# Kernel tuning notes

Hardware: AMD Instinct MI355X
Metric: run time of the kernel (lower is better)

Reference implementation:

```python
import jax, jax.numpy as jnp
import numpy as np

TEMPERATURE = 0.1
EPS = 1e-8  # torch CosineSimilarity eps


def _l2_normalize(x):
    # torch cosine sim: x / max(||x||, eps)
    n = jnp.sqrt(jnp.sum(x * x, axis=1, keepdims=True))
    return x / jnp.maximum(n, EPS)


def _pairwise_softmax(zx, zy):
    # cosine similarity matrix [N, N]: sim[i, j] = cos(zx[i], zy[j])
    sim = _l2_normalize(zx) @ _l2_normalize(zy).T  # [N, N]
    # softmax over dim=1 (columns) after temperature scaling
    return jax.nn.softmax(sim / TEMPERATURE, axis=1)


def _kl_div_mean(log_p, q):
    # torch F.kl_div(input=log_p, target=q, reduction='mean'):
    # mean over ALL elements of q * (log(q) - log_p)
    return jnp.mean(q * (jnp.log(q) - log_p))


def setup_inputs() -> dict:
    key = jax.random.key(0)
    k1, k2, k3, k4 = jax.random.split(key, 4)
    N, D = 4096, 768
    return {
        "zxs": jax.random.normal(k1, (N, D), dtype=jnp.float32),
        "zys": jax.random.normal(k2, (N, D), dtype=jnp.float32),
        "zxt": jax.random.normal(k3, (N, D), dtype=jnp.float32),
        "zyt": jax.random.normal(k4, (N, D), dtype=jnp.float32),
    }


def reference(zxs, zys, zxt, zyt):
    sim_s = _pairwise_softmax(zxs, zys)  # [N, N]
    sim_t = _pairwise_softmax(zxt, zyt)  # [N, N]
    loss_s = _kl_div_mean(jnp.log(sim_s), jax.lax.stop_gradient(sim_t))
    loss_t = _kl_div_mean(jnp.log(sim_t), jax.lax.stop_gradient(sim_s))
    return (loss_s, loss_t)
```

## Files before the change

kernel.cpp:

```cpp
#include <hip/hip_runtime.h>
#include <hip/hip_bf16.h>

#define N 4096
#define D 768
#define NK 24

typedef float f32x4 __attribute__((ext_vector_type(4)));
typedef unsigned long u64x2 __attribute__((ext_vector_type(2)));

typedef __attribute__((address_space(3))) unsigned int as3_uint;
typedef const __attribute__((address_space(1))) unsigned int as1_uint;

__device__ __forceinline__ void gload16(const void* g, void* l) {
    __builtin_amdgcn_global_load_lds((as1_uint*)g, (as3_uint*)l, 16, 0, 0);
}


__global__ __launch_bounds__(256) void norm4(const float* __restrict__ x0,
                                             const float* __restrict__ x1,
                                             const float* __restrict__ x2,
                                             const float* __restrict__ x3,
                                             unsigned char* __restrict__ o) {
    int a = blockIdx.y;
    const float* x = (a == 0) ? x0 : (a == 1) ? x1 : (a == 2) ? x2 : x3;
    unsigned char* out = o + (size_t)a * N * D;
    int i0 = blockIdx.x * 32;
    __shared__ __align__(16) unsigned char tile[24576];
    int t = threadIdx.x, lane = t & 63, w = t >> 6;

    for (int rr = 0; rr < 8; ++rr) {
        int R = i0 + w * 8 + rr;
        const f32x4* xr = (const f32x4*)(x + (size_t)R * D);
        f32x4 v0 = xr[lane * 2], v1 = xr[lane * 2 + 1];
        f32x4 v2 = {}, v3 = {};
        if (lane < 32) { v2 = xr[128 + lane * 2]; v3 = xr[128 + lane * 2 + 1]; }
        float ss = v0[0]*v0[0] + v0[1]*v0[1] + v0[2]*v0[2] + v0[3]*v0[3]
                 + v1[0]*v1[0] + v1[1]*v1[1] + v1[2]*v1[2] + v1[3]*v1[3]
                 + v2[0]*v2[0] + v2[1]*v2[1] + v2[2]*v2[2] + v2[3]*v2[3]
                 + v3[0]*v3[0] + v3[1]*v3[1] + v3[2]*v3[2] + v3[3]*v3[3];
        #pragma unroll
        for (int m = 1; m < 64; m <<= 1) ss += __shfl_xor(ss, m);
        float s = 1.0f / fmaxf(sqrtf(ss), 1e-8f);

        {
            unsigned int wlo = __builtin_amdgcn_cvt_pk_fp8_f32(v0[0]*s, v0[1]*s, 0, false) & 0xffff;
            unsigned int whi = __builtin_amdgcn_cvt_pk_fp8_f32(v0[2]*s, v0[3]*s, 0, false) & 0xffff;
            unsigned int w0 = wlo | (whi << 16);
            wlo = __builtin_amdgcn_cvt_pk_fp8_f32(v1[0]*s, v1[1]*s, 0, false) & 0xffff;
            whi = __builtin_amdgcn_cvt_pk_fp8_f32(v1[2]*s, v1[3]*s, 0, false) & 0xffff;
            unsigned int w1 = wlo | (whi << 16);
            int g = lane;
            int off = (g >> 2) * 1024 + ((R & 15) + ((g & 3) << 4)) * 16 + (((R >> 4) & 1) << 3);
            *(uint2*)(tile + off) = make_uint2(w0, w1);
        }
        if (lane < 32) {
            unsigned int wlo = __builtin_amdgcn_cvt_pk_fp8_f32(v2[0]*s, v2[1]*s, 0, false) & 0xffff;
            unsigned int whi = __builtin_amdgcn_cvt_pk_fp8_f32(v2[2]*s, v2[3]*s, 0, false) & 0xffff;
            unsigned int w0 = wlo | (whi << 16);
            wlo = __builtin_amdgcn_cvt_pk_fp8_f32(v3[0]*s, v3[1]*s, 0, false) & 0xffff;
            whi = __builtin_amdgcn_cvt_pk_fp8_f32(v3[2]*s, v3[3]*s, 0, false) & 0xffff;
            unsigned int w1 = wlo | (whi << 16);
            int g = 64 + lane;
            int off = (g >> 2) * 1024 + ((R & 15) + ((g & 3) << 4)) * 16 + (((R >> 4) & 1) << 3);
            *(uint2*)(tile + off) = make_uint2(w0, w1);
        }
    }
    __syncthreads();
    unsigned char* dst = out + (size_t)(i0 >> 5) * 24576;
    #pragma unroll
    for (int i = 0; i < 6; ++i)
        ((int4*)dst)[t + i * 256] = ((const int4*)tile)[t + i * 256];
}


__global__ __launch_bounds__(256, 2) void fused_gemm(
        const unsigned char* __restrict__ Xs, const unsigned char* __restrict__ Ys,
        const unsigned char* __restrict__ Xt, const unsigned char* __restrict__ Yt,
        float* __restrict__ partial) {
    __shared__ __align__(16) char smem[32768];
    const int t = threadIdx.x;
    const int jb = blockIdx.x, ib = blockIdx.y;
    const int i0 = ib * 128;
    const int lane = t & 63, wid = t >> 6;
    const int wm = wid >> 1, wn = wid & 1;

    f32x4 acc_s[4][4] = {};
    f32x4 acc_t[4][4] = {};

    const size_t srcA = ((size_t)(ib * 4 + (t >> 6))) * 24576 + (size_t)(t & 63) * 16;
    const size_t srcB = ((size_t)(jb * 4 + (t >> 6))) * 24576 + (size_t)(t & 63) * 16;
    const unsigned char* gAs = Xs + srcA;
    const unsigned char* gAt = Xt + srcA;
    const unsigned char* gBs = Ys + srcB;
    const unsigned char* gBt = Yt + srcB;

    char* cur = smem;
    char* nxt = smem + 16384;
    const int sdst = t * 16;

    gload16(gAs, cur + sdst);
    gload16(gBs, cur + 8192 + sdst);
    gload16(gAt, cur + 4096 + sdst);
    gload16(gBt, cur + 12288 + sdst);
    gAs += 1024; gBs += 1024; gAt += 1024; gBt += 1024;

    const int offA = wm * 2048 + lane * 16;
    const int offB = 8192 + wn * 2048 + lane * 16;

    #pragma unroll 1
    for (int kt = 0; kt < NK - 1; ++kt) {
        asm volatile("s_waitcnt vmcnt(2)" ::: "memory");
        __builtin_amdgcn_s_barrier();
        u64x2 a01 = *(const u64x2*)(cur + offA);
        u64x2 a23 = *(const u64x2*)(cur + offA + 1024);
        u64x2 b01 = *(const u64x2*)(cur + offB);
        u64x2 b23 = *(const u64x2*)(cur + offB + 1024);
        gload16(gAs, nxt + sdst);
        gload16(gBs, nxt + 8192 + sdst);
        gAs += 1024; gBs += 1024;
        {
            long a[4] = {(long)a01[0], (long)a01[1], (long)a23[0], (long)a23[1]};
            long b[4] = {(long)b01[0], (long)b01[1], (long)b23[0], (long)b23[1]};
            __builtin_amdgcn_s_setprio(1);
            #pragma unroll
            for (int m = 0; m < 4; ++m)
                #pragma unroll
                for (int n = 0; n < 4; ++n)
                    acc_s[m][n] = __builtin_amdgcn_mfma_f32_16x16x32_fp8_fp8(a[m], b[n], acc_s[m][n], 0, 0, 0);
            __builtin_amdgcn_s_setprio(0);
        }

        asm volatile("s_waitcnt vmcnt(2)" ::: "memory");
        __builtin_amdgcn_s_barrier();
        a01 = *(const u64x2*)(cur + 4096 + offA);
        a23 = *(const u64x2*)(cur + 4096 + offA + 1024);
        b01 = *(const u64x2*)(cur + 4096 + offB);
        b23 = *(const u64x2*)(cur + 4096 + offB + 1024);
        gload16(gAt, nxt + 4096 + sdst);
        gload16(gBt, nxt + 12288 + sdst);
        gAt += 1024; gBt += 1024;
        {
            long a[4] = {(long)a01[0], (long)a01[1], (long)a23[0], (long)a23[1]};
            long b[4] = {(long)b01[0], (long)b01[1], (long)b23[0], (long)b23[1]};
            __builtin_amdgcn_s_setprio(1);
            #pragma unroll
            for (int m = 0; m < 4; ++m)
                #pragma unroll
                for (int n = 0; n < 4; ++n)
                    acc_t[m][n] = __builtin_amdgcn_mfma_f32_16x16x32_fp8_fp8(a[m], b[n], acc_t[m][n], 0, 0, 0);
            __builtin_amdgcn_s_setprio(0);
        }

        char* tmp = cur; cur = nxt; nxt = tmp;
    }

    asm volatile("s_waitcnt vmcnt(2)" ::: "memory");
    __builtin_amdgcn_s_barrier();
    {
        u64x2 a01 = *(const u64x2*)(cur + offA);
        u64x2 a23 = *(const u64x2*)(cur + offA + 1024);
        u64x2 b01 = *(const u64x2*)(cur + offB);
        u64x2 b23 = *(const u64x2*)(cur + offB + 1024);
        long a[4] = {(long)a01[0], (long)a01[1], (long)a23[0], (long)a23[1]};
        long b[4] = {(long)b01[0], (long)b01[1], (long)b23[0], (long)b23[1]};
        __builtin_amdgcn_s_setprio(1);
        #pragma unroll
        for (int m = 0; m < 4; ++m)
            #pragma unroll
            for (int n = 0; n < 4; ++n)
                acc_s[m][n] = __builtin_amdgcn_mfma_f32_16x16x32_fp8_fp8(a[m], b[n], acc_s[m][n], 0, 0, 0);
        __builtin_amdgcn_s_setprio(0);
    }
    asm volatile("s_waitcnt vmcnt(0)" ::: "memory");
    __builtin_amdgcn_s_barrier();
    {
        u64x2 a01 = *(const u64x2*)(cur + 4096 + offA);
        u64x2 a23 = *(const u64x2*)(cur + 4096 + offA + 1024);
        u64x2 b01 = *(const u64x2*)(cur + 4096 + offB);
        u64x2 b23 = *(const u64x2*)(cur + 4096 + offB + 1024);
        long a[4] = {(long)a01[0], (long)a01[1], (long)a23[0], (long)a23[1]};
        long b[4] = {(long)b01[0], (long)b01[1], (long)b23[0], (long)b23[1]};
        __builtin_amdgcn_s_setprio(1);
        #pragma unroll
        for (int m = 0; m < 4; ++m)
            #pragma unroll
            for (int n = 0; n < 4; ++n)
                acc_t[m][n] = __builtin_amdgcn_mfma_f32_16x16x32_fp8_fp8(a[m], b[n], acc_t[m][n], 0, 0, 0);
        __builtin_amdgcn_s_setprio(0);
    }

    __syncthreads();
    float* part = (float*)smem;
    int g = lane >> 4, cl = lane & 15;

    #pragma unroll
    for (int m = 0; m < 4; ++m) {
        float st[4][4];
        #pragma unroll
        for (int r = 0; r < 4; ++r) { st[r][0] = 0.f; st[r][1] = 0.f; st[r][2] = 0.f; st[r][3] = 0.f; }
        #pragma unroll
        for (int n = 0; n < 4; ++n)
            #pragma unroll
            for (int r = 0; r < 4; ++r) {
                float ls = 10.0f * acc_s[m][n][r];
                float lt = 10.0f * acc_t[m][n][r];
                float es = __expf(ls - 10.0f);
                float et = __expf(lt - 10.0f);
                st[r][0] += es;
                st[r][1] += et;
                st[r][2] += es * (ls - lt);
                st[r][3] += et * (lt - ls);
            }
        #pragma unroll
        for (int r = 0; r < 4; ++r)
            #pragma unroll
            for (int s = 0; s < 4; ++s) {
                float v = st[r][s];
                v += __shfl_xor(v, 1);
                v += __shfl_xor(v, 2);
                v += __shfl_xor(v, 4);
                v += __shfl_xor(v, 8);
                st[r][s] = v;
            }
        if (cl == 0) {
            int row = wm * 64 + m * 16 + g * 4;
            #pragma unroll
            for (int r = 0; r < 4; ++r)
                #pragma unroll
                for (int s = 0; s < 4; ++s)
                    part[(wn * 128 + row + r) * 4 + s] = st[r][s];
        }
    }
    __syncthreads();
    #pragma unroll
    for (int q = 0; q < 2; ++q) {
        int idx = t + q * 256;
        int row = idx >> 2, s = idx & 3;
        float v = part[(0 * 128 + row) * 4 + s] + part[(1 * 128 + row) * 4 + s];
        partial[((size_t)jb * N + (i0 + row)) * 4 + s] = v;
    }
}

__global__ __launch_bounds__(256) void reduce_rows(const float* __restrict__ partial,
                                                   float* __restrict__ blocksum) {
    int row = blockIdx.x * 256 + threadIdx.x;
    float zs = 0.f, zt = 0.f, ws = 0.f, wt = 0.f;
    for (int jb = 0; jb < 32; ++jb) {
        const float* p = partial + ((size_t)jb * N + row) * 4;
        zs += p[0]; zt += p[1]; ws += p[2]; wt += p[3];
    }
    float ls_row = wt / zt - logf(zt) + logf(zs);
    float lt_row = ws / zs - logf(zs) + logf(zt);
    #pragma unroll
    for (int m = 1; m < 64; m <<= 1) {
        ls_row += __shfl_xor(ls_row, m);
        lt_row += __shfl_xor(lt_row, m);
    }
    __shared__ float rs[4], rt[4];
    int lane = threadIdx.x & 63, wid = threadIdx.x >> 6;
    if (lane == 0) { rs[wid] = ls_row; rt[wid] = lt_row; }
    __syncthreads();
    if (threadIdx.x == 0) {
        blocksum[blockIdx.x * 2]     = rs[0] + rs[1] + rs[2] + rs[3];
        blocksum[blockIdx.x * 2 + 1] = rt[0] + rt[1] + rt[2] + rt[3];
    }
}

__global__ void final_reduce(const float* __restrict__ blocksum, float* __restrict__ out) {
    float a = 0.f, b = 0.f;
    if (threadIdx.x < 16) { a = blocksum[threadIdx.x * 2]; b = blocksum[threadIdx.x * 2 + 1]; }
    #pragma unroll
    for (int m = 1; m < 16; m <<= 1) { a += __shfl_xor(a, m); b += __shfl_xor(b, m); }
    if (threadIdx.x == 0) {
        const float inv = 1.0f / 16777216.0f;
        out[0] = a * inv;
        out[1] = b * inv;
    }
}

extern "C" void kernel_launch(void* const* d_in, const int* in_sizes, int n_in,
                              void* d_out, int out_size, void* d_ws, size_t ws_size,
                              hipStream_t stream) {
    const float* zxs = (const float*)d_in[0];
    const float* zys = (const float*)d_in[1];
    const float* zxt = (const float*)d_in[2];
    const float* zyt = (const float*)d_in[3];

    char* ws = (char*)d_ws;
    const size_t A = (size_t)N * D;
    unsigned char* nb = (unsigned char*)ws;
    float* partial  = (float*)(ws + 4 * A);
    float* blocksum = (float*)(ws + 4 * A + (size_t)32 * N * 4 * sizeof(float));

    norm4<<<dim3(N / 32, 4), 256, 0, stream>>>(zxs, zys, zxt, zyt, nb);

    const unsigned char* Xs = nb;
    const unsigned char* Ys = nb + A;
    const unsigned char* Xt = nb + 2 * A;
    const unsigned char* Yt = nb + 3 * A;
    fused_gemm<<<dim3(32, 32), 256, 0, stream>>>(Xs, Ys, Xt, Yt, partial);

    reduce_rows<<<16, 256, 0, stream>>>(partial, blocksum);
    final_reduce<<<1, 64, 0, stream>>>(blocksum, (float*)d_out);
}
```

Baseline: 64.02 us.

## Double k-step staging per barrier and use recursive-halving shuffle reduction

The GEMM main loop now stages two K-chunks for both student and teacher pairs per iteration in a 64KB double buffer. This halves the number of barriers and issues eight async global-to-LDS loads ahead of compute. The epilogue replaces the 16 independent 4-step butterfly reductions with a recursive-halving transpose-reduce, so every lane writes one value instead of lane 0 writing sixteen. The doubled LDS per block (64KB with launch bounds of 2) may reduce occupancy, and an extra barrier per iteration is added.

```diff
diff --git a/kernel.cpp b/kernel.cpp
--- a/kernel.cpp
+++ b/kernel.cpp
@@ -3,7 +3,7 @@
 
 #define N 4096
 #define D 768
-#define NK 24
+#define NK2 12
 
 typedef float f32x4 __attribute__((ext_vector_type(4)));
 typedef unsigned long u64x2 __attribute__((ext_vector_type(2)));
@@ -77,7 +77,7 @@
         const unsigned char* __restrict__ Xs, const unsigned char* __restrict__ Ys,
         const unsigned char* __restrict__ Xt, const unsigned char* __restrict__ Yt,
         float* __restrict__ partial) {
-    __shared__ __align__(16) char smem[32768];
+    __shared__ __align__(16) char smem[65536];
     const int t = threadIdx.x;
     const int jb = blockIdx.x, ib = blockIdx.y;
     const int i0 = ib * 128;
@@ -87,155 +87,121 @@
     f32x4 acc_s[4][4] = {};
     f32x4 acc_t[4][4] = {};
 
-    const size_t srcA = ((size_t)(ib * 4 + (t >> 6))) * 24576 + (size_t)(t & 63) * 16;
-    const size_t srcB = ((size_t)(jb * 4 + (t >> 6))) * 24576 + (size_t)(t & 63) * 16;
+    const size_t srcA = ((size_t)(ib * 4 + wid)) * 24576 + (size_t)(t & 63) * 16;
+    const size_t srcB = ((size_t)(jb * 4 + wid)) * 24576 + (size_t)(t & 63) * 16;
     const unsigned char* gAs = Xs + srcA;
     const unsigned char* gAt = Xt + srcA;
     const unsigned char* gBs = Ys + srcB;
     const unsigned char* gBt = Yt + srcB;
 
     char* cur = smem;
-    char* nxt = smem + 16384;
+    char* nxt = smem + 32768;
     const int sdst = t * 16;
 
-    gload16(gAs, cur + sdst);
-    gload16(gBs, cur + 8192 + sdst);
-    gload16(gAt, cur + 4096 + sdst);
-    gload16(gBt, cur + 12288 + sdst);
-    gAs += 1024; gBs += 1024; gAt += 1024; gBt += 1024;
+    #define ISSUE8(dst, k)  do {                                                 \
+        int _off = (k) * 2048;                                                   \
+        gload16(gAs + _off,        (dst) + sdst);                                \
+        gload16(gAs + _off + 1024, (dst) + sdst + 4096);                         \
+        gload16(gBs + _off,        (dst) + 16384 + sdst);                        \
+        gload16(gBs + _off + 1024, (dst) + 16384 + sdst + 4096);                 \
+        gload16(gAt + _off,        (dst) + 8192 + sdst);                         \
+        gload16(gAt + _off + 1024, (dst) + 8192 + sdst + 4096);                  \
+        gload16(gBt + _off,        (dst) + 24576 + sdst);                        \
+        gload16(gBt + _off + 1024, (dst) + 24576 + sdst + 4096);                 \
+    } while (0)
+
+    ISSUE8(cur, 0);
 
     const int offA = wm * 2048 + lane * 16;
-    const int offB = 8192 + wn * 2048 + lane * 16;
+    const int offB = 16384 + wn * 2048 + lane * 16;
 
     #pragma unroll 1
-    for (int kt = 0; kt < NK - 1; ++kt) {
-        asm volatile("s_waitcnt vmcnt(2)" ::: "memory");
+    for (int k = 0; k < NK2; ++k) {
+        if (k < NK2 - 1) {
+            ISSUE8(nxt, k + 1);
+            asm volatile("s_waitcnt vmcnt(8)" ::: "memory");
+        } else {
+            asm volatile("s_waitcnt vmcnt(0)" ::: "memory");
+        }
         __builtin_amdgcn_s_barrier();
-        u64x2 a01 = *(const u64x2*)(cur + offA);
-        u64x2 a23 = *(const u64x2*)(cur + offA + 1024);
-        u64x2 b01 = *(const u64x2*)(cur + offB);
-        u64x2 b23 = *(const u64x2*)(cur + offB + 1024);
-        gload16(gAs, nxt + sdst);
-        gload16(gBs, nxt + 8192 + sdst);
-        gAs += 1024; gBs += 1024;
-        {
-            long a[4] = {(long)a01[0], (long)a01[1], (long)a23[0], (long)a23[1]};
-            long b[4] = {(long)b01[0], (long)b01[1], (long)b23[0], (long)b23[1]};
+
+        #pragma unroll
+        for (int kk = 0; kk < 2; ++kk) {
+            const char* c = cur + kk * 4096;
+            u64x2 as01 = *(const u64x2*)(c + offA);
+            u64x2 as23 = *(const u64x2*)(c + offA + 1024);
+            u64x2 bs01 = *(const u64x2*)(c + offB);
+            u64x2 bs23 = *(const u64x2*)(c + offB + 1024);
+            u64x2 at01 = *(const u64x2*)(c + 8192 + offA);
+            u64x2 at23 = *(const u64x2*)(c + 8192 + offA + 1024);
+            u64x2 bt01 = *(const u64x2*)(c + 8192 + offB);
+            u64x2 bt23 = *(const u64x2*)(c + 8192 + offB + 1024);
+            long a_s[4] = {(long)as01[0], (long)as01[1], (long)as23[0], (long)as23[1]};
+            long b_s[4] = {(long)bs01[0], (long)bs01[1], (long)bs23[0], (long)bs23[1]};
+            long a_t[4] = {(long)at01[0], (long)at01[1], (long)at23[0], (long)at23[1]};
+            long b_t[4] = {(long)bt01[0], (long)bt01[1], (long)bt23[0], (long)bt23[1]};
             __builtin_amdgcn_s_setprio(1);
             #pragma unroll
             for (int m = 0; m < 4; ++m)
                 #pragma unroll
                 for (int n = 0; n < 4; ++n)
-                    acc_s[m][n] = __builtin_amdgcn_mfma_f32_16x16x32_fp8_fp8(a[m], b[n], acc_s[m][n], 0, 0, 0);
-            __builtin_amdgcn_s_setprio(0);
-        }
-
-        asm volatile("s_waitcnt vmcnt(2)" ::: "memory");
-        __builtin_amdgcn_s_barrier();
-        a01 = *(const u64x2*)(cur + 4096 + offA);
-        a23 = *(const u64x2*)(cur + 4096 + offA + 1024);
-        b01 = *(const u64x2*)(cur + 4096 + offB);
-        b23 = *(const u64x2*)(cur + 4096 + offB + 1024);
-        gload16(gAt, nxt + 4096 + sdst);
-        gload16(gBt, nxt + 12288 + sdst);
-        gAt += 1024; gBt += 1024;
-        {
-            long a[4] = {(long)a01[0], (long)a01[1], (long)a23[0], (long)a23[1]};
-            long b[4] = {(long)b01[0], (long)b01[1], (long)b23[0], (long)b23[1]};
-            __builtin_amdgcn_s_setprio(1);
+                    acc_s[m][n] = __builtin_amdgcn_mfma_f32_16x16x32_fp8_fp8(a_s[m], b_s[n], acc_s[m][n], 0, 0, 0);
             #pragma unroll
             for (int m = 0; m < 4; ++m)
                 #pragma unroll
                 for (int n = 0; n < 4; ++n)
-                    acc_t[m][n] = __builtin_amdgcn_mfma_f32_16x16x32_fp8_fp8(a[m], b[n], acc_t[m][n], 0, 0, 0);
+                    acc_t[m][n] = __builtin_amdgcn_mfma_f32_16x16x32_fp8_fp8(a_t[m], b_t[n], acc_t[m][n], 0, 0, 0);
             __builtin_amdgcn_s_setprio(0);
         }
 
+        __builtin_amdgcn_s_barrier();
         char* tmp = cur; cur = nxt; nxt = tmp;
     }
-
-    asm volatile("s_waitcnt vmcnt(2)" ::: "memory");
-    __builtin_amdgcn_s_barrier();
-    {
-        u64x2 a01 = *(const u64x2*)(cur + offA);
-        u64x2 a23 = *(const u64x2*)(cur + offA + 1024);
-        u64x2 b01 = *(const u64x2*)(cur + offB);
-        u64x2 b23 = *(const u64x2*)(cur + offB + 1024);
-        long a[4] = {(long)a01[0], (long)a01[1], (long)a23[0], (long)a23[1]};
-        long b[4] = {(long)b01[0], (long)b01[1], (long)b23[0], (long)b23[1]};
-        __builtin_amdgcn_s_setprio(1);
-        #pragma unroll
-        for (int m = 0; m < 4; ++m)
-            #pragma unroll
-            for (int n = 0; n < 4; ++n)
-                acc_s[m][n] = __builtin_amdgcn_mfma_f32_16x16x32_fp8_fp8(a[m], b[n], acc_s[m][n], 0, 0, 0);
-        __builtin_amdgcn_s_setprio(0);
-    }
-    asm volatile("s_waitcnt vmcnt(0)" ::: "memory");
-    __builtin_amdgcn_s_barrier();
-    {
-        u64x2 a01 = *(const u64x2*)(cur + 4096 + offA);
-        u64x2 a23 = *(const u64x2*)(cur + 4096 + offA + 1024);
-        u64x2 b01 = *(const u64x2*)(cur + 4096 + offB);
-        u64x2 b23 = *(const u64x2*)(cur + 4096 + offB + 1024);
-        long a[4] = {(long)a01[0], (long)a01[1], (long)a23[0], (long)a23[1]};
-        long b[4] = {(long)b01[0], (long)b01[1], (long)b23[0], (long)b23[1]};
-        __builtin_amdgcn_s_setprio(1);
-        #pragma unroll
-        for (int m = 0; m < 4; ++m)
-            #pragma unroll
-            for (int n = 0; n < 4; ++n)
-                acc_t[m][n] = __builtin_amdgcn_mfma_f32_16x16x32_fp8_fp8(a[m], b[n], acc_t[m][n], 0, 0, 0);
-        __builtin_amdgcn_s_setprio(0);
-    }
+    #undef ISSUE8
 
     __syncthreads();
     float* part = (float*)smem;
-    int g = lane >> 4, cl = lane & 15;
+    const int g = lane >> 4, cl = lane & 15;
+    const int idx = ((cl & 1) << 3) | ((cl & 2) << 1) | ((cl & 4) >> 1) | ((cl & 8) >> 3);
+    const int rsel = idx >> 2, ssel = idx & 3;
+    const int rowbase = wm * 64 + g * 4 + rsel;
 
     #pragma unroll
     for (int m = 0; m < 4; ++m) {
-        float st[4][4];
-        #pragma unroll
-        for (int r = 0; r < 4; ++r) { st[r][0] = 0.f; st[r][1] = 0.f; st[r][2] = 0.f; st[r][3] = 0.f; }
+        float v[16];
+        #pragma unroll
+        for (int i = 0; i < 16; ++i) v[i] = 0.f;
         #pragma unroll
         for (int n = 0; n < 4; ++n)
             #pragma unroll
-            for (int r = 0; r < 4; ++r) {
-                float ls = 10.0f * acc_s[m][n][r];
-                float lt = 10.0f * acc_t[m][n][r];
+            for (int rr = 0; rr < 4; ++rr) {
+                float ls = 10.0f * acc_s[m][n][rr];
+                float lt = 10.0f * acc_t[m][n][rr];
                 float es = __expf(ls - 10.0f);
                 float et = __expf(lt - 10.0f);
-                st[r][0] += es;
-                st[r][1] += et;
-                st[r][2] += es * (ls - lt);
-                st[r][3] += et * (lt - ls);
+                v[rr * 4 + 0] += es;
+                v[rr * 4 + 1] += et;
+                v[rr * 4 + 2] += es * (ls - lt);
+                v[rr * 4 + 3] += et * (lt - ls);
             }
         #pragma unroll
-        for (int r = 0; r < 4; ++r)
-            #pragma unroll
-            for (int s = 0; s < 4; ++s) {
-                float v = st[r][s];
-                v += __shfl_xor(v, 1);
-                v += __shfl_xor(v, 2);
-                v += __shfl_xor(v, 4);
-                v += __shfl_xor(v, 8);
-                st[r][s] = v;
+        for (int stage = 0; stage < 4; ++stage) {
+            const int msk = 1 << stage, half = 8 >> stage;
+            const bool hi = (lane & msk) != 0;
+            #pragma unroll
+            for (int i = 0; i < half; ++i) {
+                float send = hi ? v[i] : v[i + half];
+                float recv = __shfl_xor(send, msk);
+                v[i] = (hi ? v[i + half] : v[i]) + recv;
             }
-        if (cl == 0) {
-            int row = wm * 64 + m * 16 + g * 4;
-            #pragma unroll
-            for (int r = 0; r < 4; ++r)
-                #pragma unroll
-                for (int s = 0; s < 4; ++s)
-                    part[(wn * 128 + row + r) * 4 + s] = st[r][s];
-        }
+        }
+        part[(wn * 128 + rowbase + m * 16) * 4 + ssel] = v[0];
     }
     __syncthreads();
     #pragma unroll
     for (int q = 0; q < 2; ++q) {
-        int idx = t + q * 256;
-        int row = idx >> 2, s = idx & 3;
+        int idx2 = t + q * 256;
+        int row = idx2 >> 2, s = idx2 & 3;
         float v = part[(0 * 128 + row) * 4 + s] + part[(1 * 128 + row) * 4 + s];
         partial[((size_t)jb * N + (i0 + row)) * 4 + s] = v;
     }
```

Result: slower. 95.47 us (+49.1%).

## Switch GEMM to 16x16x128 scaled FP8 MFMA with new operand layout

Applied to the files above, without the earlier changes.

Replaces the 16x16x32 fp8 MFMA with the gfx950 mfma_scale 16x16x128 f8f6f4 instruction (unit scales), so each instruction covers four times the K depth. The normalize kernel's packed fp8 layout is reorganized to match the wider operand fragments. The GEMM now runs the student and teacher products as two sequential passes with 6 larger K chunks each, doubling shared memory to 64KB. This is meant to cut MFMA issue count and loop or barrier overhead, at the cost of more LDS per block, which may reduce occupancy, and less interleaving between the two products.

```diff
diff --git a/kernel.cpp b/kernel.cpp
--- a/kernel.cpp
+++ b/kernel.cpp
@@ -3,10 +3,10 @@
 
 #define N 4096
 #define D 768
-#define NK 24
+#define NC 6
 
 typedef float f32x4 __attribute__((ext_vector_type(4)));
-typedef unsigned long u64x2 __attribute__((ext_vector_type(2)));
+typedef int v8i __attribute__((ext_vector_type(8)));
 
 typedef __attribute__((address_space(3))) unsigned int as3_uint;
 typedef const __attribute__((address_space(1))) unsigned int as1_uint;
@@ -42,6 +42,7 @@
         for (int m = 1; m < 64; m <<= 1) ss += __shfl_xor(ss, m);
         float s = 1.0f / fmaxf(sqrtf(ss), 1e-8f);
 
+        int lrg = (R >> 4) & 1;
         {
             unsigned int wlo = __builtin_amdgcn_cvt_pk_fp8_f32(v0[0]*s, v0[1]*s, 0, false) & 0xffff;
             unsigned int whi = __builtin_amdgcn_cvt_pk_fp8_f32(v0[2]*s, v0[3]*s, 0, false) & 0xffff;
@@ -50,7 +51,8 @@
             whi = __builtin_amdgcn_cvt_pk_fp8_f32(v1[2]*s, v1[3]*s, 0, false) & 0xffff;
             unsigned int w1 = wlo | (whi << 16);
             int g = lane;
-            int off = (g >> 2) * 1024 + ((R & 15) + ((g & 3) << 4)) * 16 + (((R >> 4) & 1) << 3);
+            int off = (lrg * 6 + (g >> 4)) * 2048 + ((g >> 1) & 1) * 1024
+                    + ((R & 15) + 16 * ((g & 15) >> 2)) * 16 + (g & 1) * 8;
             *(uint2*)(tile + off) = make_uint2(w0, w1);
         }
         if (lane < 32) {
@@ -61,7 +63,8 @@
             whi = __builtin_amdgcn_cvt_pk_fp8_f32(v3[2]*s, v3[3]*s, 0, false) & 0xffff;
             unsigned int w1 = wlo | (whi << 16);
             int g = 64 + lane;
-            int off = (g >> 2) * 1024 + ((R & 15) + ((g & 3) << 4)) * 16 + (((R >> 4) & 1) << 3);
+            int off = (lrg * 6 + (g >> 4)) * 2048 + ((g >> 1) & 1) * 1024
+                    + ((R & 15) + 16 * ((g & 15) >> 2)) * 16 + (g & 1) * 8;
             *(uint2*)(tile + off) = make_uint2(w0, w1);
         }
     }
@@ -72,12 +75,78 @@
         ((int4*)dst)[t + i * 256] = ((const int4*)tile)[t + i * 256];
 }
 
+__device__ __forceinline__ void gemm_pass(const unsigned char* __restrict__ A,
+                                          const unsigned char* __restrict__ B,
+                                          char* smem, int ib, int jb, int t,
+                                          f32x4 (&acc)[4][4]) {
+    const int lane = t & 63, w = t >> 6;
+    const int wm = w >> 1, wn = w & 1;
+
+    const unsigned char* gA = A + (size_t)((ib * 8 + 2 * w) * 6) * 2048 + lane * 16;
+    const unsigned char* gB = B + (size_t)((jb * 8 + 2 * w) * 6) * 2048 + lane * 16;
+    char* cur = smem;
+    char* nxt = smem + 32768;
+    const int sd = w * 4096 + lane * 16;
+
+    #define ISSUE(dst, c)  do {                                                  \
+        const unsigned char* _a = gA + (c) * 2048;                               \
+        gload16(_a,         (dst) + sd);                                         \
+        gload16(_a + 1024,  (dst) + sd + 1024);                                  \
+        gload16(_a + 12288, (dst) + sd + 2048);                                  \
+        gload16(_a + 13312, (dst) + sd + 3072);                                  \
+        const unsigned char* _b = gB + (c) * 2048;                               \
+        gload16(_b,         (dst) + 16384 + sd);                                 \
+        gload16(_b + 1024,  (dst) + 16384 + sd + 1024);                          \
+        gload16(_b + 12288, (dst) + 16384 + sd + 2048);                          \
+        gload16(_b + 13312, (dst) + 16384 + sd + 3072);                          \
+    } while (0)
+
+    ISSUE(cur, 0);
+
+    #pragma unroll 1
+    for (int c = 0; c < NC; ++c) {
+        if (c < NC - 1) {
+            ISSUE(nxt, c + 1);
+            asm volatile("s_waitcnt vmcnt(8)" ::: "memory");
+        } else {
+            asm volatile("s_waitcnt vmcnt(0)" ::: "memory");
+        }
+        __builtin_amdgcn_s_barrier();
+
+        v8i a[4], b[4];
+        #pragma unroll
+        for (int m = 0; m < 4; ++m) {
+            const char* p = cur + (wm * 4 + m) * 2048 + lane * 16;
+            int4 lo = *(const int4*)p;
+            int4 hi = *(const int4*)(p + 1024);
+            a[m] = (v8i){lo.x, lo.y, lo.z, lo.w, hi.x, hi.y, hi.z, hi.w};
+        }
+        #pragma unroll
+        for (int n = 0; n < 4; ++n) {
+            const char* p = cur + 16384 + (wn * 4 + n) * 2048 + lane * 16;
+            int4 lo = *(const int4*)p;
+            int4 hi = *(const int4*)(p + 1024);
+            b[n] = (v8i){lo.x, lo.y, lo.z, lo.w, hi.x, hi.y, hi.z, hi.w};
+        }
+        __builtin_amdgcn_s_setprio(1);
+        #pragma unroll
+        for (int m = 0; m < 4; ++m)
+            #pragma unroll
+            for (int n = 0; n < 4; ++n)
+                acc[m][n] = __builtin_amdgcn_mfma_scale_f32_16x16x128_f8f6f4(
+                    a[m], b[n], acc[m][n], 0, 0, 0, 127, 0, 127);
+        __builtin_amdgcn_s_setprio(0);
+        __builtin_amdgcn_s_barrier();
+        char* tmp = cur; cur = nxt; nxt = tmp;
+    }
+    #undef ISSUE
+}
 
 __global__ __launch_bounds__(256, 2) void fused_gemm(
         const unsigned char* __restrict__ Xs, const unsigned char* __restrict__ Ys,
         const unsigned char* __restrict__ Xt, const unsigned char* __restrict__ Yt,
         float* __restrict__ partial) {
-    __shared__ __align__(16) char smem[32768];
+    __shared__ __align__(16) char smem[65536];
     const int t = threadIdx.x;
     const int jb = blockIdx.x, ib = blockIdx.y;
     const int i0 = ib * 128;
@@ -87,107 +156,8 @@
     f32x4 acc_s[4][4] = {};
     f32x4 acc_t[4][4] = {};
 
-    const size_t srcA = ((size_t)(ib * 4 + (t >> 6))) * 24576 + (size_t)(t & 63) * 16;
-    const size_t srcB = ((size_t)(jb * 4 + (t >> 6))) * 24576 + (size_t)(t & 63) * 16;
-    const unsigned char* gAs = Xs + srcA;
-    const unsigned char* gAt = Xt + srcA;
-    const unsigned char* gBs = Ys + srcB;
-    const unsigned char* gBt = Yt + srcB;
-
-    char* cur = smem;
-    char* nxt = smem + 16384;
-    const int sdst = t * 16;
-
-    gload16(gAs, cur + sdst);
-    gload16(gBs, cur + 8192 + sdst);
-    gload16(gAt, cur + 4096 + sdst);
-    gload16(gBt, cur + 12288 + sdst);
-    gAs += 1024; gBs += 1024; gAt += 1024; gBt += 1024;
-
-    const int offA = wm * 2048 + lane * 16;
-    const int offB = 8192 + wn * 2048 + lane * 16;
-
-    #pragma unroll 1
-    for (int kt = 0; kt < NK - 1; ++kt) {
-        asm volatile("s_waitcnt vmcnt(2)" ::: "memory");
-        __builtin_amdgcn_s_barrier();
-        u64x2 a01 = *(const u64x2*)(cur + offA);
-        u64x2 a23 = *(const u64x2*)(cur + offA + 1024);
-        u64x2 b01 = *(const u64x2*)(cur + offB);
-        u64x2 b23 = *(const u64x2*)(cur + offB + 1024);
-        gload16(gAs, nxt + sdst);
-        gload16(gBs, nxt + 8192 + sdst);
-        gAs += 1024; gBs += 1024;
-        {
-            long a[4] = {(long)a01[0], (long)a01[1], (long)a23[0], (long)a23[1]};
-            long b[4] = {(long)b01[0], (long)b01[1], (long)b23[0], (long)b23[1]};
-            __builtin_amdgcn_s_setprio(1);
-            #pragma unroll
-            for (int m = 0; m < 4; ++m)
-                #pragma unroll
-                for (int n = 0; n < 4; ++n)
-                    acc_s[m][n] = __builtin_amdgcn_mfma_f32_16x16x32_fp8_fp8(a[m], b[n], acc_s[m][n], 0, 0, 0);
-            __builtin_amdgcn_s_setprio(0);
-        }
-
-        asm volatile("s_waitcnt vmcnt(2)" ::: "memory");
-        __builtin_amdgcn_s_barrier();
-        a01 = *(const u64x2*)(cur + 4096 + offA);
-        a23 = *(const u64x2*)(cur + 4096 + offA + 1024);
-        b01 = *(const u64x2*)(cur + 4096 + offB);
-        b23 = *(const u64x2*)(cur + 4096 + offB + 1024);
-        gload16(gAt, nxt + 4096 + sdst);
-        gload16(gBt, nxt + 12288 + sdst);
-        gAt += 1024; gBt += 1024;
-        {
-            long a[4] = {(long)a01[0], (long)a01[1], (long)a23[0], (long)a23[1]};
-            long b[4] = {(long)b01[0], (long)b01[1], (long)b23[0], (long)b23[1]};
-            __builtin_amdgcn_s_setprio(1);
-            #pragma unroll
-            for (int m = 0; m < 4; ++m)
-                #pragma unroll
-                for (int n = 0; n < 4; ++n)
-                    acc_t[m][n] = __builtin_amdgcn_mfma_f32_16x16x32_fp8_fp8(a[m], b[n], acc_t[m][n], 0, 0, 0);
-            __builtin_amdgcn_s_setprio(0);
-        }
-
-        char* tmp = cur; cur = nxt; nxt = tmp;
-    }
-
-    asm volatile("s_waitcnt vmcnt(2)" ::: "memory");
-    __builtin_amdgcn_s_barrier();
-    {
-        u64x2 a01 = *(const u64x2*)(cur + offA);
-        u64x2 a23 = *(const u64x2*)(cur + offA + 1024);
-        u64x2 b01 = *(const u64x2*)(cur + offB);
-        u64x2 b23 = *(const u64x2*)(cur + offB + 1024);
-        long a[4] = {(long)a01[0], (long)a01[1], (long)a23[0], (long)a23[1]};
-        long b[4] = {(long)b01[0], (long)b01[1], (long)b23[0], (long)b23[1]};
-        __builtin_amdgcn_s_setprio(1);
-        #pragma unroll
-        for (int m = 0; m < 4; ++m)
-            #pragma unroll
-            for (int n = 0; n < 4; ++n)
-                acc_s[m][n] = __builtin_amdgcn_mfma_f32_16x16x32_fp8_fp8(a[m], b[n], acc_s[m][n], 0, 0, 0);
-        __builtin_amdgcn_s_setprio(0);
-    }
-    asm volatile("s_waitcnt vmcnt(0)" ::: "memory");
-    __builtin_amdgcn_s_barrier();
-    {
-        u64x2 a01 = *(const u64x2*)(cur + 4096 + offA);
-        u64x2 a23 = *(const u64x2*)(cur + 4096 + offA + 1024);
-        u64x2 b01 = *(const u64x2*)(cur + 4096 + offB);
-        u64x2 b23 = *(const u64x2*)(cur + 4096 + offB + 1024);
-        long a[4] = {(long)a01[0], (long)a01[1], (long)a23[0], (long)a23[1]};
-        long b[4] = {(long)b01[0], (long)b01[1], (long)b23[0], (long)b23[1]};
-        __builtin_amdgcn_s_setprio(1);
-        #pragma unroll
-        for (int m = 0; m < 4; ++m)
-            #pragma unroll
-            for (int n = 0; n < 4; ++n)
-                acc_t[m][n] = __builtin_amdgcn_mfma_f32_16x16x32_fp8_fp8(a[m], b[n], acc_t[m][n], 0, 0, 0);
-        __builtin_amdgcn_s_setprio(0);
-    }
+    gemm_pass(Xs, Ys, smem, ib, jb, t, acc_s);
+    gemm_pass(Xt, Yt, smem, ib, jb, t, acc_t);
 
     __syncthreads();
     float* part = (float*)smem;
```

Result: faster. 61.72 us (-3.6%).
